# Kernel tuning notes

Hardware: AMD Instinct MI355X
Metric: run time of the kernel (lower is better)

The kernel has to match this reference:

```python
import jax, jax.numpy as jnp
import numpy as np

NPOINT, RADIUS, NSAMPLE = 1024, 0.2, 32
BN_EPS = 1e-5


def fps(xyz_bn3, npoint):
    # xyz_bn3: (B, N, 3) -> (B, npoint) int32 indices; starts from point 0 like the CUDA ext.
    def one(x):
        N = x.shape[0]
        def step(carry, _):
            dist, last = carry
            d = jnp.sum((x - x[last]) ** 2, axis=-1)
            dist = jnp.minimum(dist, d)
            nxt = jnp.argmax(dist).astype(jnp.int32)
            return (dist, nxt), nxt
        init = (jnp.full((N,), 1e10, dtype=x.dtype), jnp.int32(0))
        _, rest = jax.lax.scan(step, init, None, length=npoint - 1)
        return jnp.concatenate([jnp.zeros((1,), jnp.int32), rest])
    return jax.vmap(one)(xyz_bn3)


def ball_query(radius, nsample, xyz, new_xyz):
    # xyz: (B, N, 3), new_xyz: (B, S, 3) -> (B, S, nsample) int32
    # First nsample points within radius; pad slots with the first found index.
    N = xyz.shape[1]
    d2 = jnp.sum((new_xyz[:, :, None, :] - xyz[:, None, :, :]) ** 2, axis=-1)  # (B,S,N)
    ar = jnp.arange(N, dtype=jnp.int32)
    cand = jnp.where(d2 <= radius * radius, ar, N)
    idx = jnp.sort(cand, axis=-1)[..., :nsample]
    first = idx[..., :1]
    return jnp.where(idx == N, first, idx)


def group(features, idx):
    # features: (B, C, N), idx: (B, S, K) -> (B, C, S, K)
    return jax.vmap(lambda f, i: f[:, i])(features, idx)


def conv_bn_relu(x, w, b, g, bt, rm, rv):
    # x: (B, Cin, S, K); 1x1 conv + eval-mode BatchNorm + ReLU
    y = jnp.einsum('oc,bcsk->bosk', w, x) + b[:, None, None]
    y = g[:, None, None] * (y - rm[:, None, None]) * jax.lax.rsqrt(rv[:, None, None] + BN_EPS) + bt[:, None, None]
    return jax.nn.relu(y)


def setup_inputs() -> dict:
    key = jax.random.key(0)
    ks = jax.random.split(key, 16)
    B, N, D = 8, 4096, 64
    mlp = [64, 64, 128]
    cin = 3 + D
    inp = {
        'xyz': jax.random.uniform(ks[0], (B, 3, N), dtype=jnp.float32),
        'points': jax.random.normal(ks[1], (B, D, N), dtype=jnp.float32),
    }
    last = cin
    kidx = 2
    for i, co in enumerate(mlp):
        inp[f'w{i}'] = jax.random.normal(ks[kidx], (co, last), dtype=jnp.float32) * (1.0 / np.sqrt(last)); kidx += 1
        inp[f'b{i}'] = jax.random.normal(ks[kidx], (co,), dtype=jnp.float32) * 0.01; kidx += 1
        inp[f'g{i}'] = jax.random.uniform(ks[kidx], (co,), dtype=jnp.float32) + 0.5; kidx += 1
        inp[f'bt{i}'] = jax.random.normal(ks[kidx], (co,), dtype=jnp.float32) * 0.01; kidx += 1
        inp[f'rm{i}'] = jnp.zeros((co,), dtype=jnp.float32)
        inp[f'rv{i}'] = jnp.ones((co,), dtype=jnp.float32)
        last = co
    return inp


def reference(xyz, points, w0, b0, g0, bt0, rm0, rv0, w1, b1, g1, bt1, rm1, rv1, w2, b2, g2, bt2, rm2, rv2):
    xyz_t = jnp.transpose(xyz, (0, 2, 1))  # (B, N, 3)
    fps_idx = fps(xyz_t, NPOINT)  # (B, S)
    new_xyz = jax.vmap(lambda f, i: f[:, i])(xyz, fps_idx)  # (B, 3, S)
    idx = ball_query(RADIUS, NSAMPLE, xyz_t, jnp.transpose(new_xyz, (0, 2, 1)))  # (B, S, K)
    grouped_xyz = group(xyz, idx) - new_xyz[..., None]  # (B, 3, S, K)
    grouped_pts = group(points, idx)  # (B, D, S, K)
    feat = jnp.concatenate([grouped_xyz, grouped_pts], axis=1)  # (B, 3+D, S, K)
    feat = conv_bn_relu(feat, w0, b0, g0, bt0, rm0, rv0)
    feat = conv_bn_relu(feat, w1, b1, g1, bt1, rm1, rv1)
    feat = conv_bn_relu(feat, w2, b2, g2, bt2, rm2, rv2)
    new_features = jnp.max(feat, axis=-1)  # (B, 128, S)
    return new_xyz, new_features
```

## Files before the change

### kernel.cpp

```cpp
#include <hip/hip_runtime.h>
#include <cstdint>
#include <cstddef>

#define NPOINT 1024
#define NSAMPLE 32
#define BATCH 8
#define NPTS 4096
#define DFEAT 64
#define CIN 67
#define C1 64
#define C2 64
#define C3 128
#define BN_EPS 1e-5f

__device__ __forceinline__ float wave64_max_bcast(float v) {
    int x;
    x = __builtin_amdgcn_update_dpp(0, __float_as_int(v), 0x111, 0xf, 0xf, true);
    v = fmaxf(v, __int_as_float(x));
    x = __builtin_amdgcn_update_dpp(0, __float_as_int(v), 0x112, 0xf, 0xf, true);
    v = fmaxf(v, __int_as_float(x));
    x = __builtin_amdgcn_update_dpp(0, __float_as_int(v), 0x114, 0xf, 0xf, true);
    v = fmaxf(v, __int_as_float(x));
    x = __builtin_amdgcn_update_dpp(0, __float_as_int(v), 0x118, 0xf, 0xf, true);
    v = fmaxf(v, __int_as_float(x));
    x = __builtin_amdgcn_update_dpp(0, __float_as_int(v), 0x142, 0xf, 0xf, true);
    v = fmaxf(v, __int_as_float(x));
    x = __builtin_amdgcn_update_dpp(0, __float_as_int(v), 0x143, 0xf, 0xf, true);
    v = fmaxf(v, __int_as_float(x));
    return __int_as_float(__builtin_amdgcn_readlane(__float_as_int(v), 63));
}

__global__ __launch_bounds__(512) void fps_kernel(const float* __restrict__ xyz,
                                                  float* __restrict__ dout) {
    const int b = blockIdx.x;
    const float* xb = xyz + (size_t)b * 3 * NPTS;
    float* ox = dout + (size_t)b * 3 * NPOINT;

    __shared__ float sx[NPTS], sy[NPTS], sz[NPTS];
    __shared__ unsigned long long redk[2][8];

    const int t = threadIdx.x;
    for (int j = t; j < NPTS; j += 512) {
        sx[j] = xb[j];
        sy[j] = xb[NPTS + j];
        sz[j] = xb[2 * NPTS + j];
    }
    __syncthreads();

    constexpr int PT = NPTS / 512;
    float px[PT], py[PT], pz[PT], dist[PT];
    const int base = t * PT;
#pragma unroll
    for (int u = 0; u < PT; ++u) {
        px[u] = sx[base + u];
        py[u] = sy[base + u];
        pz[u] = sz[base + u];
        dist[u] = 1e10f;
    }

    int last = 0;
    if (t == 0) {
        ox[0] = sx[0];
        ox[NPOINT] = sy[0];
        ox[2 * NPOINT] = sz[0];
    }

    for (int s = 1; s < NPOINT; ++s) {
        const float cx = sx[last], cy = sy[last], cz = sz[last];
        float bv = 0.0f;
#pragma unroll
        for (int u = 0; u < PT; ++u) {
            float dx = __fsub_rn(px[u], cx);
            float dy = __fsub_rn(py[u], cy);
            float dz = __fsub_rn(pz[u], cz);
            float d = __fadd_rn(__fadd_rn(__fmul_rn(dx, dx), __fmul_rn(dy, dy)),
                                __fmul_rn(dz, dz));
            float nd = fminf(dist[u], d);
            dist[u] = nd;
            bv = fmaxf(bv, nd);
        }
        const float wmax = wave64_max_bcast(bv);
        int li = 0;
        if (bv == wmax) {
#pragma unroll
            for (int u = PT - 1; u >= 0; --u)
                if (dist[u] == wmax) li = base + u;
        }
        const unsigned long long m = __ballot(bv == wmax);
        const int fl = __ffsll(m) - 1;
        const int wbi = __builtin_amdgcn_readlane(li, fl);

        const int wv = t >> 6;
        if ((t & 63) == 0) {
            redk[s & 1][wv] =
                ((unsigned long long)__float_as_uint(wmax) << 32) |
                (unsigned)(0xFFFFFFFFu - (unsigned)wbi);
        }
        __syncthreads();
        unsigned long long gk = redk[s & 1][0];
#pragma unroll
        for (int w = 1; w < 8; ++w) {
            unsigned long long k2 = redk[s & 1][w];
            if (k2 > gk) gk = k2;
        }
        last = (int)(0xFFFFFFFFu - (unsigned)(gk & 0xFFFFFFFFull));
        if (t == 0) {
            ox[s] = sx[last];
            ox[NPOINT + s] = sy[last];
            ox[2 * NPOINT + s] = sz[last];
        }
    }
}

__global__ __launch_bounds__(256) void transpose_pts(const float* __restrict__ pts,
                                                     float* __restrict__ ptsT) {
    __shared__ float tile[64][65];
    const int b = blockIdx.x / (NPTS / 64);
    const int n0 = (blockIdx.x % (NPTS / 64)) * 64;
    const int t = threadIdx.x;
    const int nl = t & 63, cq = t >> 6;
    const float* pb = pts + (size_t)b * DFEAT * NPTS;
#pragma unroll
    for (int i = 0; i < 16; ++i) {
        int c = i * 4 + cq;
        tile[c][nl] = pb[(size_t)c * NPTS + n0 + nl];
    }
    __syncthreads();
    float* ob = ptsT + (size_t)b * NPTS * DFEAT;
    const int cl = t & 63, nq = t >> 6;
#pragma unroll
    for (int i = 0; i < 16; ++i) {
        int n = i * 4 + nq;
        ob[(size_t)(n0 + n) * DFEAT + cl] = tile[cl][n];
    }
}

__global__ __launch_bounds__(256) void ballquery_kernel(const float* __restrict__ xyz,
                                                        const float* __restrict__ dout,
                                                        int* __restrict__ idx) {
    const int wv = threadIdx.x >> 6, lane = threadIdx.x & 63;
    const int sg = blockIdx.x * 4 + wv;
    const int b = sg / NPOINT, s = sg % NPOINT;
    const float* xb = xyz + (size_t)b * 3 * NPTS;
    const float* nx = dout + (size_t)b * 3 * NPOINT;
    const float cx = nx[s], cy = nx[NPOINT + s], cz = nx[2 * NPOINT + s];
    int* ob = idx + (size_t)sg * NSAMPLE;
    const float r2 = 0.04f;

    int cnt = 0;
    int first = -1;
    for (int tch = 0; tch < NPTS / 64 && cnt < NSAMPLE; ++tch) {
        const int j = tch * 64 + lane;
        float dx = __fsub_rn(cx, xb[j]);
        float dy = __fsub_rn(cy, xb[NPTS + j]);
        float dz = __fsub_rn(cz, xb[2 * NPTS + j]);
        float d2 = __fadd_rn(__fadd_rn(__fmul_rn(dx, dx), __fmul_rn(dy, dy)),
                             __fmul_rn(dz, dz));
        unsigned long long mask = __ballot(d2 <= r2);
        while (mask && cnt < NSAMPLE) {
            int bit = __builtin_ctzll(mask);
            int pj = tch * 64 + bit;
            if (cnt == 0) first = pj;
            if (lane == 0) ob[cnt] = pj;
            cnt++;
            mask &= mask - 1;
        }
    }
    if (lane == 0) {
        for (int r = cnt; r < NSAMPLE; ++r) ob[r] = first;
    }
}

template <int TRANSPOSED>
__global__ __launch_bounds__(256) void mlp_kernel(
    const float* __restrict__ xyz, const float* __restrict__ pts,
    const int* __restrict__ idx, const float* __restrict__ dnew,
    const float* __restrict__ w0, const float* __restrict__ b0,
    const float* __restrict__ g0, const float* __restrict__ bt0,
    const float* __restrict__ rm0, const float* __restrict__ rv0,
    const float* __restrict__ w1, const float* __restrict__ b1,
    const float* __restrict__ g1, const float* __restrict__ bt1,
    const float* __restrict__ rm1, const float* __restrict__ rv1,
    const float* __restrict__ w2, const float* __restrict__ b2,
    const float* __restrict__ g2, const float* __restrict__ bt2,
    const float* __restrict__ rm2, const float* __restrict__ rv2,
    float* __restrict__ outf) {
    __shared__ float ylds[64][256];
    const int t = threadIdx.x;
    const int k = t & 31, sl = t >> 5;
    const int b = blockIdx.x >> 7;
    const int s = (blockIdx.x & 127) * 8 + sl;
    const int p = idx[((size_t)(b * NPOINT + s)) * NSAMPLE + k];

    const float* xb = xyz + (size_t)b * 3 * NPTS;
    const float* nx = dnew + (size_t)b * 3 * NPOINT;

    float x[CIN];
    x[0] = xb[p] - nx[s];
    x[1] = xb[NPTS + p] - nx[NPOINT + s];
    x[2] = xb[2 * NPTS + p] - nx[2 * NPOINT + s];
    if (TRANSPOSED) {
        const float* pb = pts + ((size_t)b * NPTS + p) * DFEAT;
#pragma unroll
        for (int c = 0; c < DFEAT; ++c) x[3 + c] = pb[c];
    } else {
        const float* pb = pts + (size_t)b * DFEAT * NPTS + p;
#pragma unroll
        for (int c = 0; c < DFEAT; ++c) x[3 + c] = pb[(size_t)c * NPTS];
    }

    for (int o = 0; o < C1; ++o) {
        float acc = 0.f;
#pragma unroll
        for (int c = 0; c < CIN; ++c) acc = fmaf(w0[o * CIN + c], x[c], acc);
        float sc = g0[o] * rsqrtf(rv0[o] + BN_EPS);
        float y = fmaf(sc, acc + b0[o] - rm0[o], bt0[o]);
        ylds[o][t] = fmaxf(y, 0.f);
    }
    __syncthreads();
    float x1[C1];
#pragma unroll
    for (int c = 0; c < C1; ++c) x1[c] = ylds[c][t];
    __syncthreads();

    for (int o = 0; o < C2; ++o) {
        float acc = 0.f;
#pragma unroll
        for (int c = 0; c < C1; ++c) acc = fmaf(w1[o * C1 + c], x1[c], acc);
        float sc = g1[o] * rsqrtf(rv1[o] + BN_EPS);
        float y = fmaf(sc, acc + b1[o] - rm1[o], bt1[o]);
        ylds[o][t] = fmaxf(y, 0.f);
    }
    __syncthreads();
    float x2[C2];
#pragma unroll
    for (int c = 0; c < C2; ++c) x2[c] = ylds[c][t];

    float* ob = outf + (size_t)b * C3 * NPOINT;
    for (int o = 0; o < C3; ++o) {
        float acc = 0.f;
#pragma unroll
        for (int c = 0; c < C2; ++c) acc = fmaf(w2[o * C2 + c], x2[c], acc);
        float sc = g2[o] * rsqrtf(rv2[o] + BN_EPS);
        float y = fmaf(sc, acc + b2[o] - rm2[o], bt2[o]);
        float v = fmaxf(y, 0.f);
#pragma unroll
        for (int m = 16; m >= 1; m >>= 1) v = fmaxf(v, __shfl_xor(v, m, 32));
        if (k == 0) ob[(size_t)o * NPOINT + s] = v;
    }
}

extern "C" void kernel_launch(void* const* d_in, const int* in_sizes, int n_in,
                              void* d_out, int out_size, void* d_ws, size_t ws_size,
                              hipStream_t stream) {
    const float* xyz = (const float*)d_in[0];
    const float* pts = (const float*)d_in[1];
    const float* w0 = (const float*)d_in[2];
    const float* b0 = (const float*)d_in[3];
    const float* g0 = (const float*)d_in[4];
    const float* bt0 = (const float*)d_in[5];
    const float* rm0 = (const float*)d_in[6];
    const float* rv0 = (const float*)d_in[7];
    const float* w1 = (const float*)d_in[8];
    const float* b1 = (const float*)d_in[9];
    const float* g1 = (const float*)d_in[10];
    const float* bt1 = (const float*)d_in[11];
    const float* rm1 = (const float*)d_in[12];
    const float* rv1 = (const float*)d_in[13];
    const float* w2 = (const float*)d_in[14];
    const float* b2 = (const float*)d_in[15];
    const float* g2 = (const float*)d_in[16];
    const float* bt2 = (const float*)d_in[17];
    const float* rm2 = (const float*)d_in[18];
    const float* rv2 = (const float*)d_in[19];

    float* out = (float*)d_out;
    float* outf = out + (size_t)BATCH * 3 * NPOINT;

    const size_t idx_bytes = (size_t)BATCH * NPOINT * NSAMPLE * sizeof(int);
    const size_t idx_pad = (idx_bytes + 255) & ~(size_t)255;
    const size_t ptsT_bytes = (size_t)BATCH * NPTS * DFEAT * sizeof(float);
    int* idx = (int*)d_ws;
    float* ptsT = (float*)((char*)d_ws + idx_pad);
    const bool useT = ws_size >= idx_pad + ptsT_bytes;

    fps_kernel<<<BATCH, 512, 0, stream>>>(xyz, out);
    if (useT) transpose_pts<<<BATCH * (NPTS / 64), 256, 0, stream>>>(pts, ptsT);
    ballquery_kernel<<<BATCH * NPOINT / 4, 256, 0, stream>>>(xyz, out, idx);
    if (useT) {
        mlp_kernel<1><<<BATCH * NPOINT / 8, 256, 0, stream>>>(
            xyz, ptsT, idx, out, w0, b0, g0, bt0, rm0, rv0, w1, b1, g1, bt1, rm1,
            rv1, w2, b2, g2, bt2, rm2, rv2, outf);
    } else {
        mlp_kernel<0><<<BATCH * NPOINT / 8, 256, 0, stream>>>(
            xyz, pts, idx, out, w0, b0, g0, bt0, rm0, rv0, w1, b1, g1, bt1, rm1,
            rv1, w2, b2, g2, bt2, rm2, rv2, outf);
    }
}
```

Baseline: 966.7 us.

## Restructure FPS with packed-f32 math, fewer waves, coordinate broadcast; split MLP accumulators

The FPS kernel drops to 256 threads with 16 points per thread and computes distances with packed v_pk_add/v_pk_mul instructions. It no longer stages the whole point cloud in LDS: each wave broadcasts the winning coordinates through readlane plus a small shared buffer, which removes the dependent LDS lookup of the selected point on every iteration. Separately, the MLP dot products now use four independent accumulators to shorten FMA dependency chains, which changes the floating-point summation order. FPS is a serial 1023-step loop run by only 8 blocks and likely dominates the runtime, so shortening each step is the main goal; the cost is more registers per thread and fewer parallel waves.

```diff
diff --git a/kernel.cpp b/kernel.cpp
--- a/kernel.cpp
+++ b/kernel.cpp
@@ -13,6 +13,19 @@
 #define C3 128
 #define BN_EPS 1e-5f
 
+typedef float f32x2 __attribute__((ext_vector_type(2)));
+
+__device__ __forceinline__ f32x2 pk_add(f32x2 a, f32x2 b) {
+    f32x2 d;
+    asm("v_pk_add_f32 %0, %1, %2" : "=v"(d) : "v"(a), "v"(b));
+    return d;
+}
+__device__ __forceinline__ f32x2 pk_mul(f32x2 a, f32x2 b) {
+    f32x2 d;
+    asm("v_pk_mul_f32 %0, %1, %2" : "=v"(d) : "v"(a), "v"(b));
+    return d;
+}
+
 __device__ __forceinline__ float wave64_max_bcast(float v) {
     int x;
     x = __builtin_amdgcn_update_dpp(0, __float_as_int(v), 0x111, 0xf, 0xf, true);
@@ -30,84 +43,109 @@
     return __int_as_float(__builtin_amdgcn_readlane(__float_as_int(v), 63));
 }
 
-__global__ __launch_bounds__(512) void fps_kernel(const float* __restrict__ xyz,
+__global__ __launch_bounds__(256) void fps_kernel(const float* __restrict__ xyz,
                                                   float* __restrict__ dout) {
     const int b = blockIdx.x;
     const float* xb = xyz + (size_t)b * 3 * NPTS;
     float* ox = dout + (size_t)b * 3 * NPOINT;
 
-    __shared__ float sx[NPTS], sy[NPTS], sz[NPTS];
-    __shared__ unsigned long long redk[2][8];
+    __shared__ unsigned long long keys[2][4];
+    __shared__ float4 scoord[2][4];
 
     const int t = threadIdx.x;
-    for (int j = t; j < NPTS; j += 512) {
-        sx[j] = xb[j];
-        sy[j] = xb[NPTS + j];
-        sz[j] = xb[2 * NPTS + j];
-    }
-    __syncthreads();
-
-    constexpr int PT = NPTS / 512;
-    float px[PT], py[PT], pz[PT], dist[PT];
+    constexpr int PT = NPTS / 256;
+    constexpr int G = PT / 2;
     const int base = t * PT;
-#pragma unroll
-    for (int u = 0; u < PT; ++u) {
-        px[u] = sx[base + u];
-        py[u] = sy[base + u];
-        pz[u] = sz[base + u];
-        dist[u] = 1e10f;
-    }
-
-    int last = 0;
+
+    f32x2 px2[G], py2[G], pz2[G], dist2[G];
+    {
+        const float4* fx = (const float4*)(xb + base);
+        const float4* fy = (const float4*)(xb + NPTS + base);
+        const float4* fz = (const float4*)(xb + 2 * NPTS + base);
+#pragma unroll
+        for (int q = 0; q < PT / 4; ++q) {
+            float4 vx = fx[q], vy = fy[q], vz = fz[q];
+            px2[2 * q] = f32x2{vx.x, vx.y};
+            px2[2 * q + 1] = f32x2{vx.z, vx.w};
+            py2[2 * q] = f32x2{vy.x, vy.y};
+            py2[2 * q + 1] = f32x2{vy.z, vy.w};
+            pz2[2 * q] = f32x2{vz.x, vz.y};
+            pz2[2 * q + 1] = f32x2{vz.z, vz.w};
+        }
+#pragma unroll
+        for (int g = 0; g < G; ++g) dist2[g] = f32x2{1e10f, 1e10f};
+    }
+
+    float cx = xb[0], cy = xb[NPTS], cz = xb[2 * NPTS];
     if (t == 0) {
-        ox[0] = sx[0];
-        ox[NPOINT] = sy[0];
-        ox[2 * NPOINT] = sz[0];
-    }
-
+        ox[0] = cx;
+        ox[NPOINT] = cy;
+        ox[2 * NPOINT] = cz;
+    }
+
+    const int wv = t >> 6;
     for (int s = 1; s < NPOINT; ++s) {
-        const float cx = sx[last], cy = sy[last], cz = sz[last];
+        const f32x2 ncx = {-cx, -cx}, ncy = {-cy, -cy}, ncz = {-cz, -cz};
         float bv = 0.0f;
 #pragma unroll
-        for (int u = 0; u < PT; ++u) {
-            float dx = __fsub_rn(px[u], cx);
-            float dy = __fsub_rn(py[u], cy);
-            float dz = __fsub_rn(pz[u], cz);
-            float d = __fadd_rn(__fadd_rn(__fmul_rn(dx, dx), __fmul_rn(dy, dy)),
-                                __fmul_rn(dz, dz));
-            float nd = fminf(dist[u], d);
-            dist[u] = nd;
-            bv = fmaxf(bv, nd);
+        for (int g = 0; g < G; ++g) {
+            f32x2 dx = pk_add(px2[g], ncx);
+            f32x2 dy = pk_add(py2[g], ncy);
+            f32x2 dz = pk_add(pz2[g], ncz);
+            f32x2 xx = pk_mul(dx, dx);
+            f32x2 yy = pk_mul(dy, dy);
+            f32x2 zz = pk_mul(dz, dz);
+            f32x2 sm = pk_add(xx, yy);
+            f32x2 d2 = pk_add(sm, zz);
+            float n0 = fminf(dist2[g].x, d2.x);
+            float n1 = fminf(dist2[g].y, d2.y);
+            dist2[g].x = n0;
+            dist2[g].y = n1;
+            bv = fmaxf(fmaxf(bv, n0), n1);
         }
         const float wmax = wave64_max_bcast(bv);
+
         int li = 0;
+        float ccx = 0.f, ccy = 0.f, ccz = 0.f;
         if (bv == wmax) {
 #pragma unroll
-            for (int u = PT - 1; u >= 0; --u)
-                if (dist[u] == wmax) li = base + u;
+            for (int g = G - 1; g >= 0; --g) {
+                if (dist2[g].y == wmax) {
+                    li = base + 2 * g + 1;
+                    ccx = px2[g].y; ccy = py2[g].y; ccz = pz2[g].y;
+                }
+                if (dist2[g].x == wmax) {
+                    li = base + 2 * g;
+                    ccx = px2[g].x; ccy = py2[g].x; ccz = pz2[g].x;
+                }
+            }
         }
         const unsigned long long m = __ballot(bv == wmax);
-        const int fl = __ffsll(m) - 1;
+        const int fl = __builtin_ctzll(m);
         const int wbi = __builtin_amdgcn_readlane(li, fl);
-
-        const int wv = t >> 6;
+        const float wcx = __int_as_float(__builtin_amdgcn_readlane(__float_as_int(ccx), fl));
+        const float wcy = __int_as_float(__builtin_amdgcn_readlane(__float_as_int(ccy), fl));
+        const float wcz = __int_as_float(__builtin_amdgcn_readlane(__float_as_int(ccz), fl));
+
         if ((t & 63) == 0) {
-            redk[s & 1][wv] =
-                ((unsigned long long)__float_as_uint(wmax) << 32) |
-                (unsigned)(0xFFFFFFFFu - (unsigned)wbi);
+            keys[s & 1][wv] = ((unsigned long long)__float_as_uint(wmax) << 32) |
+                              (unsigned)(0xFFFFFFFFu - (unsigned)wbi);
+            scoord[s & 1][wv] = make_float4(wcx, wcy, wcz, 0.f);
         }
         __syncthreads();
-        unsigned long long gk = redk[s & 1][0];
-#pragma unroll
-        for (int w = 1; w < 8; ++w) {
-            unsigned long long k2 = redk[s & 1][w];
-            if (k2 > gk) gk = k2;
-        }
-        last = (int)(0xFFFFFFFFu - (unsigned)(gk & 0xFFFFFFFFull));
+        unsigned long long gk = keys[s & 1][0];
+        float4 gc = scoord[s & 1][0];
+#pragma unroll
+        for (int w = 1; w < 4; ++w) {
+            unsigned long long k2 = keys[s & 1][w];
+            float4 c2 = scoord[s & 1][w];
+            if (k2 > gk) { gk = k2; gc = c2; }
+        }
+        cx = gc.x; cy = gc.y; cz = gc.z;
         if (t == 0) {
-            ox[s] = sx[last];
-            ox[NPOINT + s] = sy[last];
-            ox[2 * NPOINT + s] = sz[last];
+            ox[s] = cx;
+            ox[NPOINT + s] = cy;
+            ox[2 * NPOINT + s] = cz;
         }
     }
 }
@@ -210,9 +248,19 @@
     }
 
     for (int o = 0; o < C1; ++o) {
-        float acc = 0.f;
-#pragma unroll
-        for (int c = 0; c < CIN; ++c) acc = fmaf(w0[o * CIN + c], x[c], acc);
+        const float* wr = w0 + o * CIN;
+        float a0 = 0.f, a1 = 0.f, a2 = 0.f, a3 = 0.f;
+#pragma unroll
+        for (int c = 0; c < 64; c += 4) {
+            a0 = fmaf(wr[c], x[c], a0);
+            a1 = fmaf(wr[c + 1], x[c + 1], a1);
+            a2 = fmaf(wr[c + 2], x[c + 2], a2);
+            a3 = fmaf(wr[c + 3], x[c + 3], a3);
+        }
+        a0 = fmaf(wr[64], x[64], a0);
+        a1 = fmaf(wr[65], x[65], a1);
+        a2 = fmaf(wr[66], x[66], a2);
+        float acc = (a0 + a1) + (a2 + a3);
         float sc = g0[o] * rsqrtf(rv0[o] + BN_EPS);
         float y = fmaf(sc, acc + b0[o] - rm0[o], bt0[o]);
         ylds[o][t] = fmaxf(y, 0.f);
@@ -224,9 +272,16 @@
     __syncthreads();
 
     for (int o = 0; o < C2; ++o) {
-        float acc = 0.f;
-#pragma unroll
-        for (int c = 0; c < C1; ++c) acc = fmaf(w1[o * C1 + c], x1[c], acc);
+        const float* wr = w1 + o * C1;
+        float a0 = 0.f, a1 = 0.f, a2 = 0.f, a3 = 0.f;
+#pragma unroll
+        for (int c = 0; c < C1; c += 4) {
+            a0 = fmaf(wr[c], x1[c], a0);
+            a1 = fmaf(wr[c + 1], x1[c + 1], a1);
+            a2 = fmaf(wr[c + 2], x1[c + 2], a2);
+            a3 = fmaf(wr[c + 3], x1[c + 3], a3);
+        }
+        float acc = (a0 + a1) + (a2 + a3);
         float sc = g1[o] * rsqrtf(rv1[o] + BN_EPS);
         float y = fmaf(sc, acc + b1[o] - rm1[o], bt1[o]);
         ylds[o][t] = fmaxf(y, 0.f);
@@ -238,9 +293,16 @@
 
     float* ob = outf + (size_t)b * C3 * NPOINT;
     for (int o = 0; o < C3; ++o) {
-        float acc = 0.f;
-#pragma unroll
-        for (int c = 0; c < C2; ++c) acc = fmaf(w2[o * C2 + c], x2[c], acc);
+        const float* wr = w2 + o * C2;
+        float a0 = 0.f, a1 = 0.f, a2 = 0.f, a3 = 0.f;
+#pragma unroll
+        for (int c = 0; c < C2; c += 4) {
+            a0 = fmaf(wr[c], x2[c], a0);
+            a1 = fmaf(wr[c + 1], x2[c + 1], a1);
+            a2 = fmaf(wr[c + 2], x2[c + 2], a2);
+            a3 = fmaf(wr[c + 3], x2[c + 3], a3);
+        }
+        float acc = (a0 + a1) + (a2 + a3);
         float sc = g2[o] * rsqrtf(rv2[o] + BN_EPS);
         float y = fmaf(sc, acc + b2[o] - rm2[o], bt2[o]);
         float v = fmaxf(y, 0.f);
@@ -284,7 +346,7 @@
     float* ptsT = (float*)((char*)d_ws + idx_pad);
     const bool useT = ws_size >= idx_pad + ptsT_bytes;
 
-    fps_kernel<<<BATCH, 512, 0, stream>>>(xyz, out);
+    fps_kernel<<<BATCH, 256, 0, stream>>>(xyz, out);
     if (useT) transpose_pts<<<BATCH * (NPTS / 64), 256, 0, stream>>>(pts, ptsT);
     ballquery_kernel<<<BATCH * NPOINT / 4, 256, 0, stream>>>(xyz, out, idx);
     if (useT) {
```

After: 1.321 ms. +36.7%, slower.
